# Optimization experiments

Measured on AMD Instinct MI355X. Metric: run time of the kernel, lower is better.

Reference implementation:

```python
import jax, jax.numpy as jnp
import numpy as np

EPS = 1e-5
BT_BATCH = 32       # BarlowTwinsLoss init batch_size (divides c)
BT_LAMBD = 0.005

def seg_sum(v, idx, n):
    return jax.ops.segment_sum(v, idx, num_segments=n)

def seg_mean(v, idx, n):
    s = seg_sum(v, idx, n)
    c = seg_sum(jnp.ones((v.shape[0],), v.dtype), idx, n)
    return s / jnp.maximum(c, 1.0)[:, None]

def gcn_conv(x, W, b, edge_index):
    n = x.shape[0]
    src, dst = edge_index[0], edge_index[1]
    xw = x @ W
    deg = 1.0 + seg_sum(jnp.ones(src.shape, x.dtype), dst, n)  # self-loop included
    norm = jax.lax.rsqrt(deg[src] * deg[dst])
    out = seg_sum(norm[:, None] * xw[src], dst, n) + xw / deg[:, None]
    return out + b

def barlow(z1, z2):
    # z-score with unbiased std (torch.std), then BatchNorm1d(affine=False) stats
    def std1(z):
        return (z - z.mean(0)) / jnp.std(z, axis=0, ddof=1)
    def bn(z):
        return (z - z.mean(0)) / jnp.sqrt(z.var(0) + EPS)
    a, b = bn(std1(z1)), bn(std1(z2))
    c = (a.T @ b) / BT_BATCH
    d = jnp.diagonal(c)
    on_diag = jnp.sum((d - 1.0) ** 2)
    off_diag = jnp.sum(c ** 2) - jnp.sum(d ** 2)
    return on_diag + BT_LAMBD * off_diag

def layernorm(t, g, b):
    m = t.mean(-1, keepdims=True)
    v = t.var(-1, keepdims=True)
    return g * (t - m) / jnp.sqrt(v + EPS) + b

def setup_inputs() -> dict:
    key = jax.random.key(0)
    ks = jax.random.split(key, 24)
    N, M, d, B = 50000, 10000, 128, 32
    NNZ, EG, EE = 200000, 600000, 160000
    s = 1.0 / np.sqrt(d)
    inp = {
        'x': jax.random.normal(ks[0], (N, d), jnp.float32),
        'hyperedge_feature': jax.random.normal(ks[1], (M, d), jnp.float32),
        'node_coord': jax.random.normal(ks[2], (N, 3), jnp.float32),
        'hyperedge_node_idx': jax.random.randint(ks[3], (NNZ,), 0, N),
        'hyperedge_edge_idx': jax.random.randint(ks[4], (NNZ,), 0, M),
        'node_batch_idx': jnp.sort(jax.random.randint(ks[5], (N,), 0, B)),
        'hyperedge_batch_idx': jnp.sort(jax.random.randint(ks[6], (M,), 0, B)),
        'X_X': jax.random.randint(ks[7], (2, EG), 0, N),
        'E_E': jax.random.randint(ks[8], (2, EE), 0, M),
        'num_graphs': B,
        'Wv': jax.random.normal(ks[9], (d, d), jnp.float32) * s,
        'bv': jnp.zeros((d,), jnp.float32),
        'We': jax.random.normal(ks[10], (d, d), jnp.float32) * s,
        'be': jnp.zeros((d,), jnp.float32),
        'Wx': jax.random.normal(ks[11], (d, d), jnp.float32) * s,
        'bx': jnp.zeros((d,), jnp.float32),
        'Weg': jax.random.normal(ks[12], (d, d), jnp.float32) * s,
        'beg': jnp.zeros((d,), jnp.float32),
        'ln_g': jnp.ones((d,), jnp.float32),
        'ln_b': jnp.zeros((d,), jnp.float32),
        'Wf': jax.random.normal(ks[13], (2 * d, d), jnp.float32) * (1.0 / np.sqrt(2 * d)),
        'bf': jnp.zeros((d,), jnp.float32),
    }
    return inp

def reference(x, hyperedge_feature, node_coord, hyperedge_node_idx, hyperedge_edge_idx,
              node_batch_idx, hyperedge_batch_idx, X_X, E_E, num_graphs,
              Wv, bv, We, be, Wx, bx, Weg, beg, ln_g, ln_b, Wf, bf):
    N, d = x.shape
    M = hyperedge_feature.shape[0]
    ni, ei = hyperedge_node_idx, hyperedge_edge_idx
    # E_HypergraphConv: node<->hyperedge bipartite message passing + EGNN-style coord update
    xw = x @ Wv + bv                     # [N, d]
    ew = hyperedge_feature @ We + be     # [M, d]
    e_conv = seg_mean(xw[ni], ei, M)     # hyperedge update from member nodes
    z_conv = seg_mean(ew[ei], ni, N)     # node update from incident hyperedges
    edge_coord = seg_mean(node_coord[ni], ei, M)          # [M, 3]
    rel = node_coord[ni] - edge_coord[ei]                 # [nnz, 3]
    phi = jnp.tanh(jnp.sum(xw[ni] * ew[ei], -1, keepdims=True)
                   * jax.lax.rsqrt(jnp.asarray(float(d), x.dtype)))
    update_coord = node_coord + seg_mean(rel * phi, ni, N)
    # implicit graph branches
    z_imp = gcn_conv(x, Wx, bx, X_X)
    e_imp = gcn_conv(hyperedge_feature, Weg, beg, E_E)
    bt_loss = barlow(z_imp, z_conv) + barlow(e_imp, e_conv)
    # norm -> GELU (erf, torch default) -> dropout(eval=identity) -> residual
    z = jax.nn.gelu(layernorm(z_conv, ln_g, ln_b), approximate=False) + x
    e = jax.nn.gelu(layernorm(e_conv, ln_g, ln_b), approximate=False) + hyperedge_feature
    z_graph = seg_mean(z, node_batch_idx, num_graphs)
    e_graph = seg_mean(e, hyperedge_batch_idx, num_graphs)
    graph = jnp.concatenate([z_graph, e_graph], axis=1) @ Wf + bf
    return z, e, update_coord, graph, bt_loss
```

## Files before the change

### kernel.cpp

```cpp
#include <hip/hip_runtime.h>
#include <hip/hip_bf16.h>

#define NB 32
#define GPN 448
#define GPM 80
#define RGRP 16

__device__ __forceinline__ float wave_sum(float v) {
#pragma unroll
  for (int off = 32; off; off >>= 1) v += __shfl_xor(v, off);
  return v;
}
__device__ __forceinline__ int wave_sum_i(int v) {
#pragma unroll
  for (int off = 32; off; off >>= 1) v += __shfl_xor(v, off);
  return v;
}

__device__ __forceinline__ float bf2f(unsigned short u) {
  return __uint_as_float(((unsigned int)u) << 16);
}
__device__ __forceinline__ unsigned short f2bf(float f) {
  unsigned int v = __float_as_uint(f);
  return (unsigned short)((v + 0x7FFFu + ((v >> 16) & 1u)) >> 16);
}

__global__ void count_kernel(const int* __restrict__ ni, const int* __restrict__ ei,
                             int nnz, const int* __restrict__ xx, int eg,
                             const int* __restrict__ ee, int eeN, int* cnt_n,
                             int* cnt_e, int* cnt_gx, int* cnt_ge, int* rank_pn,
                             int* rank_pe, int* rank_g, int* rank_h,
                             const float* __restrict__ coord, float* ec) {
  int i = blockIdx.x * 1024 + (int)threadIdx.x;
#pragma unroll
  for (int k = 0; k < 4; k++, i += 256) {
    if (i < nnz) {
      const int n = ni[i], e = ei[i];
      rank_pn[i] = atomicAdd(&cnt_n[n], 1);
      rank_pe[i] = atomicAdd(&cnt_e[e], 1);
      atomicAdd(&ec[e * 3 + 0], coord[n * 3 + 0]);
      atomicAdd(&ec[e * 3 + 1], coord[n * 3 + 1]);
      atomicAdd(&ec[e * 3 + 2], coord[n * 3 + 2]);
    } else if (i < nnz + eg) {
      const int j = i - nnz;
      rank_g[j] = atomicAdd(&cnt_gx[xx[eg + j]], 1);
    } else if (i < nnz + eg + eeN) {
      const int j = i - nnz - eg;
      rank_h[j] = atomicAdd(&cnt_ge[ee[eeN + j]], 1);
    }
  }
}

__device__ __forceinline__ void gemm_body(const float* __restrict__ X,
                                          const float* __restrict__ W1,
                                          const float* __restrict__ b1,
                                          unsigned short* __restrict__ out1,
                                          const float* __restrict__ W2,
                                          unsigned short* __restrict__ out2, int rows,
                                          int blk, unsigned short (*xs)[132]) {
  const int t = threadIdx.x;
  const int c4 = t & 31;
  const int rg = t >> 5;
  const int r0 = blk * 64;
#pragma unroll
  for (int i = 0; i < 8; i++) {
    const int idx = t + i * 256;
    const int row = idx >> 5, cc = idx & 31;
    const int gr = r0 + row;
    float4 v = make_float4(0.f, 0.f, 0.f, 0.f);
    if (gr < rows) v = ((const float4*)X)[(size_t)gr * 32 + cc];
    ushort4 u;
    u.x = f2bf(v.x); u.y = f2bf(v.y); u.z = f2bf(v.z); u.w = f2bf(v.w);
    *(ushort4*)&xs[row][cc * 4] = u;
  }
  __syncthreads();
  const float4* W1v = (const float4*)W1;
  const float4* W2v = (const float4*)W2;
  const float4 b4 = ((const float4*)b1)[c4];
  float4 acc1[8], acc2[8];
#pragma unroll
  for (int i = 0; i < 8; i++) {
    acc1[i] = b4;
    acc2[i] = make_float4(0.f, 0.f, 0.f, 0.f);
  }
  const int rbase = rg * 8;
#pragma unroll 2
  for (int k = 0; k < 128; k++) {
    const float4 w1 = W1v[k * 32 + c4];
    const float4 w2 = W2v[k * 32 + c4];
#pragma unroll
    for (int i = 0; i < 8; i++) {
      const float xv = bf2f(xs[rbase + i][k]);
      acc1[i].x = fmaf(xv, w1.x, acc1[i].x);
      acc1[i].y = fmaf(xv, w1.y, acc1[i].y);
      acc1[i].z = fmaf(xv, w1.z, acc1[i].z);
      acc1[i].w = fmaf(xv, w1.w, acc1[i].w);
      acc2[i].x = fmaf(xv, w2.x, acc2[i].x);
      acc2[i].y = fmaf(xv, w2.y, acc2[i].y);
      acc2[i].z = fmaf(xv, w2.z, acc2[i].z);
      acc2[i].w = fmaf(xv, w2.w, acc2[i].w);
    }
  }
#pragma unroll
  for (int i = 0; i < 8; i++) {
    const int gr = r0 + rbase + i;
    if (gr < rows) {
      ushort4 o1, o2;
      o1.x = f2bf(acc1[i].x); o1.y = f2bf(acc1[i].y);
      o1.z = f2bf(acc1[i].z); o1.w = f2bf(acc1[i].w);
      o2.x = f2bf(acc2[i].x); o2.y = f2bf(acc2[i].y);
      o2.z = f2bf(acc2[i].z); o2.w = f2bf(acc2[i].w);
      ((ushort4*)out1)[(size_t)gr * 32 + c4] = o1;
      ((ushort4*)out2)[(size_t)gr * 32 + c4] = o2;
    }
  }
}

__global__ __launch_bounds__(256) void scan_partial(
    const int* __restrict__ c0, int n0, const int* __restrict__ c1, int n1,
    const int* __restrict__ c2, int n2, const int* __restrict__ c3, int n3,
    int nb0, int nb1, int nb2, int nb3, int* __restrict__ bsums) {
  const int gb = blockIdx.x;
  const int* cnt;
  int lb, n;
  if (gb < nb0) { cnt = c0; lb = gb; n = n0; }
  else if (gb < nb0 + nb1) { cnt = c1; lb = gb - nb0; n = n1; }
  else if (gb < nb0 + nb1 + nb2) { cnt = c2; lb = gb - nb0 - nb1; n = n2; }
  else { cnt = c3; lb = gb - nb0 - nb1 - nb2; n = n3; }
  const int t = threadIdx.x;
  const int base = lb * 4096 + t * 16;
  int s = 0;
#pragma unroll
  for (int i = 0; i < 16; i++) {
    const int idx = base + i;
    if (idx < n) s += cnt[idx];
  }
  const int wsum = wave_sum_i(s);
  __shared__ int wsm[4];
  if ((t & 63) == 0) wsm[t >> 6] = wsum;
  __syncthreads();
  if (t == 0) bsums[gb] = wsm[0] + wsm[1] + wsm[2] + wsm[3];
}

__global__ void scan_bsums(const int* __restrict__ bsums, int nb0, int nb1, int nb2,
                           int nb3, int* __restrict__ bbase, int* __restrict__ totals) {
  if (threadIdx.x) return;
  int segs[4] = {nb0, nb1, nb2, nb3};
  int gb = 0;
  for (int a = 0; a < 4; a++) {
    int run = 0;
    for (int i = 0; i < segs[a]; i++) {
      bbase[gb] = run;
      run += bsums[gb];
      gb++;
    }
    totals[a] = run;
  }
}

__global__ __launch_bounds__(256) void scan_final(
    int* __restrict__ c0, int* rp0, float* rs0, float* ecd0, int n0,
    int* __restrict__ c1, int* rp1, float* rs1, float* ecd1, int n1,
    int* __restrict__ c2, int* rp2, float* rs2, float* ecd2, int n2,
    int* __restrict__ c3, int* rp3, float* rs3, float* ecd3, int n3,
    int nb0, int nb1, int nb2, int nb3, const int* __restrict__ bbase,
    const int* __restrict__ totals) {
  const int gb = blockIdx.x;
  int* cnt;
  int* rp;
  float* rs;
  float* ecd;
  int lb, n, a;
  if (gb < nb0) { cnt = c0; rp = rp0; rs = rs0; ecd = ecd0; lb = gb; n = n0; a = 0; }
  else if (gb < nb0 + nb1) { cnt = c1; rp = rp1; rs = rs1; ecd = ecd1; lb = gb - nb0; n = n1; a = 1; }
  else if (gb < nb0 + nb1 + nb2) { cnt = c2; rp = rp2; rs = rs2; ecd = ecd2; lb = gb - nb0 - nb1; n = n2; a = 2; }
  else { cnt = c3; rp = rp3; rs = rs3; ecd = ecd3; lb = gb - nb0 - nb1 - nb2; n = n3; a = 3; }
  const int t = threadIdx.x;
  const int base = lb * 4096 + t * 16;
  int vals[16];
  int s = 0;
#pragma unroll
  for (int i = 0; i < 16; i++) {
    const int idx = base + i;
    vals[i] = (idx < n) ? cnt[idx] : 0;
    s += vals[i];
  }
  __shared__ int tsum[256];
  tsum[t] = s;
  __syncthreads();
  for (int off = 1; off < 256; off <<= 1) {
    const int v = (t >= off) ? tsum[t - off] : 0;
    __syncthreads();
    tsum[t] += v;
    __syncthreads();
  }
  int run = bbase[gb] + (t ? tsum[t - 1] : 0);
#pragma unroll
  for (int i = 0; i < 16; i++) {
    const int idx = base + i;
    if (idx < n) {
      rp[idx] = run;
      if (rs) rs[idx] = rsqrtf(1.f + (float)vals[i]);
      if (ecd) {
        const float inv = 1.f / fmaxf((float)vals[i], 1.f);
        ecd[idx * 3 + 0] *= inv;
        ecd[idx * 3 + 1] *= inv;
        ecd[idx * 3 + 2] *= inv;
      }
      run += vals[i];
    }
  }
  if (t == 0 && lb == 0) rp[n] = totals[a];
}

__global__ __launch_bounds__(256) void fused_fill_gemm(
    const float* __restrict__ x, const float* __restrict__ Wv,
    const float* __restrict__ bv, unsigned short* __restrict__ xw,
    const float* __restrict__ Wx, unsigned short* __restrict__ xw2, int N, int nbGN,
    const float* __restrict__ hf, const float* __restrict__ We,
    const float* __restrict__ be, unsigned short* __restrict__ ew,
    const float* __restrict__ Weg, unsigned short* __restrict__ ew2, int M, int nbG,
    const int* __restrict__ ni, const int* __restrict__ ei, int nnz,
    const int* __restrict__ xx, int eg, const int* __restrict__ ee, int eeN,
    const int* __restrict__ rp_n, const int* __restrict__ rp_e,
    const int* __restrict__ rp_gx, const int* __restrict__ rp_ge,
    const int* __restrict__ rank_pn, const int* __restrict__ rank_pe,
    const int* __restrict__ rank_g, const int* __restrict__ rank_h, int* adj_n,
    int* adj_e, int* adj_gx, int* adj_ge, int nbFill, const int* __restrict__ nbi,
    int* cbn, const int* __restrict__ hbi, int* cbe) {
  __shared__ unsigned short xs[64][132];
  const int b = blockIdx.x;
  const int t = threadIdx.x;
  if (b < nbG) {
    if (b < nbGN)
      gemm_body(x, Wv, bv, xw, Wx, xw2, N, b, xs);
    else
      gemm_body(hf, We, be, ew, Weg, ew2, M, b - nbGN, xs);
    return;
  }
  const int fb = b - nbG;
  if (fb < nbFill) {
    int i = fb * 1024 + t;
#pragma unroll
    for (int k = 0; k < 4; k++, i += 256) {
      if (i < nnz) {
        const int n0 = ni[i], e0 = ei[i];
        adj_n[rp_n[n0] + rank_pn[i]] = e0;
        adj_e[rp_e[e0] + rank_pe[i]] = n0;
      } else if (i < nnz + eg) {
        const int j = i - nnz;
        adj_gx[rp_gx[xx[eg + j]] + rank_g[j]] = xx[j];
      } else if (i < nnz + eg + eeN) {
        const int j = i - nnz - eg;
        adj_ge[rp_ge[ee[eeN + j]] + rank_h[j]] = ee[j];
      }
    }
    return;
  }
  const bool B = (fb - nbFill) != 0;
  const int* idx = B ? hbi : nbi;
  const int nn = B ? M : N;
  int* out = B ? cbe : cbn;
  const int g = t;
  if (g >= NB) return;
  int lo = 0, hi = nn;
  while (lo < hi) { int mid = (lo + hi) >> 1; if (idx[mid] < g) lo = mid + 1; else hi = mid; }
  const int l = lo;
  lo = 0; hi = nn;
  while (lo < hi) { int mid = (lo + hi) >> 1; if (idx[mid] < g + 1) lo = mid + 1; else hi = mid; }
  out[g] = lo - l;
}

__device__ __forceinline__ void gcn_body(const unsigned short* __restrict__ xw,
                                         const int* __restrict__ rowptr,
                                         const int* __restrict__ adj,
                                         const float* __restrict__ rs,
                                         const float* __restrict__ bias,
                                         float* __restrict__ out, int n, int lb) {
  const int r = (lb * 256 + (int)threadIdx.x) >> 6;
  const int lane = threadIdx.x & 63;
  if (r >= n) return;
  const int lo = rowptr[r], hi = rowptr[r + 1];
  const float rd = rs[r];
  float2 acc = make_float2(0.f, 0.f);
  for (int base = lo; base < hi; base += 64) {
    const int mm = min(64, hi - base);
    int aj = 0;
    float rj = 0.f;
    if (base + lane < hi) {
      aj = adj[base + lane];
      rj = rs[aj];
    }
    for (int j = 0; j < mm; j++) {
      const int s = __shfl(aj, j);
      const float w = __shfl(rj, j);
      const ushort2 u = ((const ushort2*)xw)[(size_t)s * 64 + lane];
      acc.x = fmaf(w, bf2f(u.x), acc.x);
      acc.y = fmaf(w, bf2f(u.y), acc.y);
    }
  }
  const ushort2 su = ((const ushort2*)xw)[(size_t)r * 64 + lane];
  const float2 bb = ((const float2*)bias)[lane];
  float2 o;
  o.x = fmaf(rd, acc.x, fmaf(rd * rd, bf2f(su.x), bb.x));
  o.y = fmaf(rd, acc.y, fmaf(rd * rd, bf2f(su.y), bb.y));
  ((float2*)out)[(size_t)r * 64 + lane] = o;
}

__global__ __launch_bounds__(256) void fused_gathers(
    const unsigned short* __restrict__ ew, const unsigned short* __restrict__ xw,
    const float* __restrict__ coord, const float* __restrict__ ecoord,
    const int* __restrict__ rp_n, const int* __restrict__ adj_n,
    float* __restrict__ z_conv, float* __restrict__ outc, int N, int nbNode,
    const unsigned short* __restrict__ xw2, const int* __restrict__ rp_gx,
    const int* __restrict__ adj_gx, const float* __restrict__ rs_gx,
    const float* __restrict__ bx, float* __restrict__ outz, int nbGcnN,
    const unsigned short* __restrict__ ew2, const int* __restrict__ rp_ge,
    const int* __restrict__ adj_ge, const float* __restrict__ rs_ge,
    const float* __restrict__ beg, float* __restrict__ oute, int M, int nbGcnM,
    const int* __restrict__ rp_e, const int* __restrict__ adj_e,
    float* __restrict__ e_conv) {
  const int b = blockIdx.x;
  const int t = threadIdx.x;
  const int lane = t & 63;
  if (b < nbNode) {
    const int r = (b * 256 + t) >> 6;
    if (r >= N) return;
    const int lo = rp_n[r], hi = rp_n[r + 1];
    const ushort2 au = ((const ushort2*)xw)[(size_t)r * 64 + lane];
    const float2 a = make_float2(bf2f(au.x), bf2f(au.y));
    const float myc = (lane < 3) ? coord[r * 3 + lane] : 0.f;
    float2 acc = make_float2(0.f, 0.f);
    float cacc = 0.f;
    for (int base = lo; base < hi; base += 64) {
      const int mm = min(64, hi - base);
      int aj = (base + lane < hi) ? adj_n[base + lane] : 0;
      for (int j = 0; j < mm; j++) {
        const int e = __shfl(aj, j);
        const ushort2 bu = ((const ushort2*)ew)[(size_t)e * 64 + lane];
        const float2 bb = make_float2(bf2f(bu.x), bf2f(bu.y));
        acc.x += bb.x;
        acc.y += bb.y;
        const float dot = wave_sum(fmaf(a.x, bb.x, a.y * bb.y));
        const float ph = tanhf(dot * 0.08838834764831845f);
        if (lane < 3) cacc = fmaf(myc - ecoord[e * 3 + lane], ph, cacc);
      }
    }
    const float inv = 1.f / fmaxf((float)(hi - lo), 1.f);
    ((float2*)z_conv)[(size_t)r * 64 + lane] = make_float2(acc.x * inv, acc.y * inv);
    if (lane < 3) outc[r * 3 + lane] = myc + cacc * inv;
    return;
  }
  if (b < nbNode + nbGcnN) {
    gcn_body(xw2, rp_gx, adj_gx, rs_gx, bx, outz, N, b - nbNode);
    return;
  }
  if (b < nbNode + nbGcnN + nbGcnM) {
    gcn_body(ew2, rp_ge, adj_ge, rs_ge, beg, oute, M, b - nbNode - nbGcnN);
    return;
  }
  const int lb = b - nbNode - nbGcnN - nbGcnM;
  const int e = (lb * 256 + t) >> 6;
  if (e >= M) return;
  const int lo = rp_e[e], hi = rp_e[e + 1];
  float2 acc = make_float2(0.f, 0.f);
  for (int base = lo; base < hi; base += 64) {
    const int mm = min(64, hi - base);
    int aj = (base + lane < hi) ? adj_e[base + lane] : 0;
    for (int j = 0; j < mm; j++) {
      const int nidx = __shfl(aj, j);
      const ushort2 vu = ((const ushort2*)xw)[(size_t)nidx * 64 + lane];
      acc.x += bf2f(vu.x);
      acc.y += bf2f(vu.y);
    }
  }
  const float inv = 1.f / fmaxf((float)(hi - lo), 1.f);
  ((float2*)e_conv)[(size_t)e * 64 + lane] = make_float2(acc.x * inv, acc.y * inv);
}

__global__ __launch_bounds__(256) void gram_partial2(
    const float* __restrict__ Z1a, const float* __restrict__ Z2a, int na,
    float* __restrict__ parta, const float* __restrict__ Z1b,
    const float* __restrict__ Z2b, int nbm, float* __restrict__ partb,
    float* __restrict__ st, int nblkA) {
  const bool A = (int)blockIdx.x < nblkA;
  const int pid = A ? blockIdx.x : blockIdx.x - nblkA;
  const float* Z1 = A ? Z1a : Z1b;
  const float* Z2 = A ? Z2a : Z2b;
  const int n = A ? na : nbm;
  const int gparts = A ? GPN : GPM;
  float* part = (A ? parta : partb) + (size_t)pid * 16384;
  float* sum1 = st + (A ? 0 : 512);
  float* ssq1 = sum1 + 128;
  float* sum2 = sum1 + 256;
  float* ssq2 = sum1 + 384;
  __shared__ float4 s1[256], s2[256];
  const int t = threadIdx.x;
  const int ti = t >> 4, tj = t & 15;
  const int rpb = (n + gparts - 1) / gparts;
  const int lo = pid * rpb, hi = min(lo + rpb, n);
  float acc[8][8];
#pragma unroll
  for (int i = 0; i < 8; i++)
#pragma unroll
    for (int j = 0; j < 8; j++) acc[i][j] = 0.f;
  float cs = 0.f, cq = 0.f;
  const float* s1f = (const float*)s1;
  const float* s2f = (const float*)s2;
  const int c = t & 127;
  const bool low = t < 128;
  for (int rb = lo; rb < hi; rb += 8) {
    const int nr = min(8, hi - rb);
    __syncthreads();
    if (t < nr * 32) {
      const int rr = rb + (t >> 5);
      s1[t] = ((const float4*)Z1)[(size_t)rr * 32 + (t & 31)];
      s2[t] = ((const float4*)Z2)[(size_t)rr * 32 + (t & 31)];
    }
    __syncthreads();
    for (int r = 0; r < nr; r++) {
      const float4 a0 = s1[r * 32 + ti * 2], a1 = s1[r * 32 + ti * 2 + 1];
      const float4 b0 = s2[r * 32 + tj * 2], b1 = s2[r * 32 + tj * 2 + 1];
      const float av[8] = {a0.x, a0.y, a0.z, a0.w, a1.x, a1.y, a1.z, a1.w};
      const float bv[8] = {b0.x, b0.y, b0.z, b0.w, b1.x, b1.y, b1.z, b1.w};
#pragma unroll
      for (int i = 0; i < 8; i++)
#pragma unroll
        for (int j = 0; j < 8; j++) acc[i][j] = fmaf(av[i], bv[j], acc[i][j]);
      const float v = low ? s1f[r * 128 + c] : s2f[r * 128 + c];
      cs += v;
      cq = fmaf(v, v, cq);
    }
  }
  float4* P = (float4*)part;
#pragma unroll
  for (int i = 0; i < 8; i++) {
    P[(ti * 8 + i) * 32 + tj * 2] = make_float4(acc[i][0], acc[i][1], acc[i][2], acc[i][3]);
    P[(ti * 8 + i) * 32 + tj * 2 + 1] = make_float4(acc[i][4], acc[i][5], acc[i][6], acc[i][7]);
  }
  if (low) {
    atomicAdd(&sum1[c], cs);
    atomicAdd(&ssq1[c], cq);
  } else {
    atomicAdd(&sum2[c], cs);
    atomicAdd(&ssq2[c], cq);
  }
}

__global__ __launch_bounds__(256) void fused_reduce_ln(
    const float* __restrict__ parta, float* __restrict__ G1,
    const float* __restrict__ partb, float* __restrict__ G2,
    const float* __restrict__ convA, const float* __restrict__ residA,
    float* __restrict__ outA, int nA, int lnA, const float* __restrict__ convB,
    const float* __restrict__ residB, float* __restrict__ outB, int nBm,
    const float* __restrict__ g, const float* __restrict__ bvec) {
  const int b = blockIdx.x;
  const int t = threadIdx.x;
  const int NRED = (GPN / RGRP + GPM / RGRP) * 16;
  if (b < NRED) {
    const int nga = GPN / RGRP;
    const int slice = b & 15;
    const int grp = b >> 4;
    const bool A = grp < nga;
    const float* part = A ? parta : partb;
    float* G = A ? G1 : G2;
    const int g0 = (A ? grp : grp - nga) * RGRP;
    const int e = slice * 1024 + t * 4;
    float4 s = make_float4(0.f, 0.f, 0.f, 0.f);
#pragma unroll 4
    for (int p = 0; p < RGRP; p++) {
      const float4 v = *(const float4*)&part[(size_t)(g0 + p) * 16384 + e];
      s.x += v.x;
      s.y += v.y;
      s.z += v.z;
      s.w += v.w;
    }
    atomicAdd(&G[e], s.x);
    atomicAdd(&G[e + 1], s.y);
    atomicAdd(&G[e + 2], s.z);
    atomicAdd(&G[e + 3], s.w);
    return;
  }
  const int b2 = b - NRED;
  const bool A = b2 < lnA;
  const int lb = A ? b2 : b2 - lnA;
  const float* conv = A ? convA : convB;
  const float* resid = A ? residA : residB;
  float* out = A ? outA : outB;
  const int rows = A ? nA : nBm;
  const int w = (lb * 256 + t) >> 6;
  const int lane = t & 63;
  if (w >= rows) return;
  const float2 v = ((const float2*)conv)[(size_t)w * 64 + lane];
  const float m = wave_sum(v.x + v.y) * (1.f / 128.f);
  const float q = wave_sum(fmaf(v.x, v.x, v.y * v.y)) * (1.f / 128.f);
  const float rstd = rsqrtf(q - m * m + 1e-5f);
  const float2 gg = ((const float2*)g)[lane];
  const float2 bb = ((const float2*)bvec)[lane];
  const float2 rr = ((const float2*)resid)[(size_t)w * 64 + lane];
  float y0 = fmaf(gg.x, (v.x - m) * rstd, bb.x);
  float y1 = fmaf(gg.y, (v.y - m) * rstd, bb.y);
  y0 = 0.5f * y0 * (1.f + erff(y0 * 0.7071067811865476f));
  y1 = 0.5f * y1 * (1.f + erff(y1 * 0.7071067811865476f));
  float2 o;
  o.x = y0 + rr.x;
  o.y = y1 + rr.y;
  ((float2*)out)[(size_t)w * 64 + lane] = o;
}

__global__ __launch_bounds__(256) void fused_fin_pool(
    const float* __restrict__ G1, const float* __restrict__ G2,
    const float* __restrict__ st, float nA, float nB, float* outbt,
    const float* __restrict__ ZA, const int* __restrict__ bidxA, int n, int spA,
    float* poolA, const float* __restrict__ ZB, const int* __restrict__ bidxB, int m,
    float* poolB) {
  __shared__ float s1s[128], m1s[128], s2s[128], m2s[128];
  __shared__ float red[256];
  const int b = blockIdx.x;
  const int t = threadIdx.x;
  if (b < 2) {
    const bool A = b == 0;
    const float* G = A ? G1 : G2;
    const float* sum1 = st + (A ? 0 : 512);
    const float* ssq1 = sum1 + 128;
    const float* sum2 = sum1 + 256;
    const float* ssq2 = sum1 + 384;
    const float nn = A ? nA : nB;
    if (t < 128) {
      const float inv_n = 1.f / nn;
      const float bnf = (nn - 1.f) * inv_n + 1e-5f;
      float mu = sum1[t] * inv_n;
      float vu = (ssq1[t] * inv_n - mu * mu) * nn / (nn - 1.f);
      s1s[t] = rsqrtf(vu * bnf);
      m1s[t] = mu;
      mu = sum2[t] * inv_n;
      vu = (ssq2[t] * inv_n - mu * mu) * nn / (nn - 1.f);
      s2s[t] = rsqrtf(vu * bnf);
      m2s[t] = mu;
    }
    __syncthreads();
    float on = 0.f, off = 0.f;
    for (int idx = t; idx < 16384; idx += 256) {
      const int i = idx >> 7, j = idx & 127;
      const float c = s1s[i] * s2s[j] * (G[idx] - nn * m1s[i] * m2s[j]) * (1.f / 32.f);
      if (i == j) {
        const float dd = c - 1.f;
        on += dd * dd;
      } else {
        off += c * c;
      }
    }
    red[t] = on + 0.005f * off;
    __syncthreads();
    for (int s = 128; s; s >>= 1) {
      if (t < s) red[t] += red[t + s];
      __syncthreads();
    }
    if (t == 0) atomicAdd(outbt, red[0]);
    return;
  }
  const int pb = b - 2;
  const bool A = pb < spA;
  const int lb = A ? pb : pb - spA;
  const float* Z = A ? ZA : ZB;
  const int* bidx = A ? bidxA : bidxB;
  const int n2 = A ? n : m;
  float* pool = A ? poolA : poolB;
  const int c = t & 127;
  const int h = t >> 7;
  const int r0 = lb * 128 + h * 64;
  const int re = min(lb * 128 + (h + 1) * 64, n2);
  if (r0 >= n2) return;
  float acc = 0.f;
  int cur = bidx[r0];
  for (int r = r0; r < re; r++) {
    const int bb = bidx[r];
    if (bb != cur) {
      atomicAdd(&pool[cur * 128 + c], acc);
      acc = 0.f;
      cur = bb;
    }
    acc += Z[(size_t)r * 128 + c];
  }
  atomicAdd(&pool[cur * 128 + c], acc);
}

__global__ __launch_bounds__(128) void graph_gemm(
    const float* __restrict__ zg, const float* __restrict__ eg,
    const int* __restrict__ cnz, const int* __restrict__ cne,
    const float* __restrict__ Wf, const float* __restrict__ bf, float* out) {
  __shared__ float cat[256];
  const int g = blockIdx.x, t = threadIdx.x;
  cat[t] = zg[g * 128 + t] / fmaxf((float)cnz[g], 1.f);
  cat[128 + t] = eg[g * 128 + t] / fmaxf((float)cne[g], 1.f);
  __syncthreads();
  float acc = bf[t];
#pragma unroll 8
  for (int k = 0; k < 256; k++) acc = fmaf(cat[k], Wf[k * 128 + t], acc);
  out[g * 128 + t] = acc;
}

extern "C" void kernel_launch(void* const* d_in, const int* in_sizes, int n_in,
                              void* d_out, int out_size, void* d_ws, size_t ws_size,
                              hipStream_t stream) {
  const float* x = (const float*)d_in[0];
  const float* hf = (const float*)d_in[1];
  const float* coord = (const float*)d_in[2];
  const int* ni = (const int*)d_in[3];
  const int* ei = (const int*)d_in[4];
  const int* nb = (const int*)d_in[5];
  const int* hb = (const int*)d_in[6];
  const int* xx = (const int*)d_in[7];
  const int* ee = (const int*)d_in[8];
  const float* Wv = (const float*)d_in[10];
  const float* bv = (const float*)d_in[11];
  const float* We = (const float*)d_in[12];
  const float* be = (const float*)d_in[13];
  const float* Wx = (const float*)d_in[14];
  const float* bx = (const float*)d_in[15];
  const float* Weg = (const float*)d_in[16];
  const float* beg = (const float*)d_in[17];
  const float* lng = (const float*)d_in[18];
  const float* lnb = (const float*)d_in[19];
  const float* Wf = (const float*)d_in[20];
  const float* bf = (const float*)d_in[21];

  const int N = in_sizes[0] / 128;
  const int M = in_sizes[1] / 128;
  const int NNZ = in_sizes[3];
  const int EG = in_sizes[7] / 2;
  const int EE = in_sizes[8] / 2;

  float* ws = (float*)d_ws;
  size_t o = 0;
  unsigned short* xw = (unsigned short*)(ws + o);  o += (size_t)N * 64;
  unsigned short* ew = (unsigned short*)(ws + o);  o += (size_t)M * 64;
  unsigned short* xw2 = (unsigned short*)(ws + o); o += (size_t)N * 64;
  unsigned short* ew2 = (unsigned short*)(ws + o); o += (size_t)M * 64;
  int* rank_pn = (int*)(ws + o); o += NNZ;
  int* rank_pe = (int*)(ws + o); o += NNZ;
  int* rank_g = (int*)(ws + o);  o += EG;
  int* rank_h = (int*)(ws + o);  o += EE;
  float* z_conv = ws + o; o += (size_t)N * 128;
  float* e_conv = ws + o; o += (size_t)M * 128;
  float* rs_gx = ws + o;  o += N;
  float* rs_ge = ws + o;  o += M;
  const size_t fz0 = o;
  float* ecoord = ws + o; o += (size_t)M * 3;
  float* G1 = ws + o;     o += 16384;
  float* G2 = ws + o;     o += 16384;
  float* st = ws + o;     o += 1024;
  float* zg = ws + o;     o += NB * 128;
  float* eg_p = ws + o;   o += NB * 128;
  const size_t fz1 = o;
  int* wsi = (int*)(ws + o);
  size_t oi = 0;
  int* cnt_n = wsi + oi;  oi += N;
  int* cnt_e = wsi + oi;  oi += M;
  int* cnt_gx = wsi + oi; oi += N;
  int* cnt_ge = wsi + oi; oi += M;
  const size_t iz1 = oi;
  int* rp_n = wsi + oi;   oi += N + 1;
  int* rp_e = wsi + oi;   oi += M + 1;
  int* rp_gx = wsi + oi;  oi += N + 1;
  int* rp_ge = wsi + oi;  oi += M + 1;
  int* adj_n = wsi + oi;  oi += NNZ;
  int* adj_e = wsi + oi;  oi += NNZ;
  int* adj_gx = wsi + oi; oi += EG;
  int* adj_ge = wsi + oi; oi += EE;
  int* cbn = wsi + oi;    oi += NB;
  int* cbe = wsi + oi;    oi += NB;
  int* bsums = wsi + oi;  oi += 64;
  int* bbase = wsi + oi;  oi += 64;
  int* totals = wsi + oi; oi += 4;

  float* gpartA = ws;
  float* gpartB = ws + (size_t)GPN * 16384;

  float* outz = (float*)d_out;
  float* oute = outz + (size_t)N * 128;
  float* outc = oute + (size_t)M * 128;
  float* outg = outc + (size_t)N * 3;
  float* outbt = outg + NB * 128;

  hipMemsetAsync(ws + fz0, 0, (fz1 - fz0) * 4, stream);
  hipMemsetAsync(wsi, 0, iz1 * 4, stream);
  hipMemsetAsync(outbt, 0, 4, stream);

  const int tot = NNZ + EG + EE;
  const int nbCnt = (tot + 1023) >> 10;
  count_kernel<<<nbCnt, 256, 0, stream>>>(ni, ei, NNZ, xx, EG, ee, EE, cnt_n, cnt_e,
                                          cnt_gx, cnt_ge, rank_pn, rank_pe, rank_g,
                                          rank_h, coord, ecoord);

  const int nb0 = (N + 4095) >> 12, nb1 = (M + 4095) >> 12;
  const int sgrid = 2 * nb0 + 2 * nb1;
  scan_partial<<<sgrid, 256, 0, stream>>>(cnt_n, N, cnt_e, M, cnt_gx, N, cnt_ge, M,
                                          nb0, nb1, nb0, nb1, bsums);
  scan_bsums<<<1, 64, 0, stream>>>(bsums, nb0, nb1, nb0, nb1, bbase, totals);
  scan_final<<<sgrid, 256, 0, stream>>>(
      cnt_n, rp_n, nullptr, nullptr, N, cnt_e, rp_e, nullptr, ecoord, M, cnt_gx,
      rp_gx, rs_gx, nullptr, N, cnt_ge, rp_ge, rs_ge, nullptr, M, nb0, nb1, nb0, nb1,
      bbase, totals);

  const int nbGN = (N + 63) / 64, nbGM = (M + 63) / 64;
  const int nbG = nbGN + nbGM;
  const int nbFill = (tot + 1023) >> 10;
  fused_fill_gemm<<<nbG + nbFill + 2, 256, 0, stream>>>(
      x, Wv, bv, xw, Wx, xw2, N, nbGN, hf, We, be, ew, Weg, ew2, M, nbG, ni, ei, NNZ,
      xx, EG, ee, EE, rp_n, rp_e, rp_gx, rp_ge, rank_pn, rank_pe, rank_g, rank_h,
      adj_n, adj_e, adj_gx, adj_ge, nbFill, nb, cbn, hb, cbe);

  const int nbNode = (N + 3) / 4, nbGcnN = (N + 3) / 4, nbGcnM = (M + 3) / 4,
            nbHedge = (M + 3) / 4;
  fused_gathers<<<nbNode + nbGcnN + nbGcnM + nbHedge, 256, 0, stream>>>(
      ew, xw, coord, ecoord, rp_n, adj_n, z_conv, outc, N, nbNode, xw2, rp_gx, adj_gx,
      rs_gx, bx, outz, nbGcnN, ew2, rp_ge, adj_ge, rs_ge, beg, oute, M, nbGcnM, rp_e,
      adj_e, e_conv);

  gram_partial2<<<GPN + GPM, 256, 0, stream>>>(outz, z_conv, N, gpartA, oute, e_conv,
                                               M, gpartB, st, GPN);

  const int lnA = (N + 3) / 4;
  fused_reduce_ln<<<(GPN / RGRP + GPM / RGRP) * 16 + lnA + (M + 3) / 4, 256, 0,
                    stream>>>(gpartA, G1, gpartB, G2, z_conv, x, outz, N, lnA, e_conv,
                              hf, oute, M, lng, lnb);

  const int spA = (N + 127) / 128, spB = (M + 127) / 128;
  fused_fin_pool<<<2 + spA + spB, 256, 0, stream>>>(G1, G2, st, (float)N, (float)M,
                                                    outbt, outz, nb, N, spA, zg, oute,
                                                    hb, M, eg_p);

  graph_gemm<<<NB, 128, 0, stream>>>(zg, eg_p, cbn, cbe, Wf, bf, outg);
}
```

Baseline: 387.8 us.

## Use half-wave rows with 8-byte loads in gathers; compute edge coords by CSR gather

```diff
diff --git a/kernel.cpp b/kernel.cpp
--- a/kernel.cpp
+++ b/kernel.cpp
@@ -11,6 +11,11 @@
   for (int off = 32; off; off >>= 1) v += __shfl_xor(v, off);
   return v;
 }
+__device__ __forceinline__ float half_sum(float v) {
+#pragma unroll
+  for (int off = 16; off; off >>= 1) v += __shfl_xor(v, off);
+  return v;
+}
 __device__ __forceinline__ int wave_sum_i(int v) {
 #pragma unroll
   for (int off = 32; off; off >>= 1) v += __shfl_xor(v, off);
@@ -29,8 +34,7 @@
                              int nnz, const int* __restrict__ xx, int eg,
                              const int* __restrict__ ee, int eeN, int* cnt_n,
                              int* cnt_e, int* cnt_gx, int* cnt_ge, int* rank_pn,
-                             int* rank_pe, int* rank_g, int* rank_h,
-                             const float* __restrict__ coord, float* ec) {
+                             int* rank_pe, int* rank_g, int* rank_h) {
   int i = blockIdx.x * 1024 + (int)threadIdx.x;
 #pragma unroll
   for (int k = 0; k < 4; k++, i += 256) {
@@ -38,9 +42,6 @@
       const int n = ni[i], e = ei[i];
       rank_pn[i] = atomicAdd(&cnt_n[n], 1);
       rank_pe[i] = atomicAdd(&cnt_e[e], 1);
-      atomicAdd(&ec[e * 3 + 0], coord[n * 3 + 0]);
-      atomicAdd(&ec[e * 3 + 1], coord[n * 3 + 1]);
-      atomicAdd(&ec[e * 3 + 2], coord[n * 3 + 2]);
     } else if (i < nnz + eg) {
       const int j = i - nnz;
       rank_g[j] = atomicAdd(&cnt_gx[xx[eg + j]], 1);
@@ -159,22 +160,21 @@
 }
 
 __global__ __launch_bounds__(256) void scan_final(
-    int* __restrict__ c0, int* rp0, float* rs0, float* ecd0, int n0,
-    int* __restrict__ c1, int* rp1, float* rs1, float* ecd1, int n1,
-    int* __restrict__ c2, int* rp2, float* rs2, float* ecd2, int n2,
-    int* __restrict__ c3, int* rp3, float* rs3, float* ecd3, int n3,
+    int* __restrict__ c0, int* rp0, float* rs0, int n0,
+    int* __restrict__ c1, int* rp1, float* rs1, int n1,
+    int* __restrict__ c2, int* rp2, float* rs2, int n2,
+    int* __restrict__ c3, int* rp3, float* rs3, int n3,
     int nb0, int nb1, int nb2, int nb3, const int* __restrict__ bbase,
     const int* __restrict__ totals) {
   const int gb = blockIdx.x;
   int* cnt;
   int* rp;
   float* rs;
-  float* ecd;
   int lb, n, a;
-  if (gb < nb0) { cnt = c0; rp = rp0; rs = rs0; ecd = ecd0; lb = gb; n = n0; a = 0; }
-  else if (gb < nb0 + nb1) { cnt = c1; rp = rp1; rs = rs1; ecd = ecd1; lb = gb - nb0; n = n1; a = 1; }
-  else if (gb < nb0 + nb1 + nb2) { cnt = c2; rp = rp2; rs = rs2; ecd = ecd2; lb = gb - nb0 - nb1; n = n2; a = 2; }
-  else { cnt = c3; rp = rp3; rs = rs3; ecd = ecd3; lb = gb - nb0 - nb1 - nb2; n = n3; a = 3; }
+  if (gb < nb0) { cnt = c0; rp = rp0; rs = rs0; lb = gb; n = n0; a = 0; }
+  else if (gb < nb0 + nb1) { cnt = c1; rp = rp1; rs = rs1; lb = gb - nb0; n = n1; a = 1; }
+  else if (gb < nb0 + nb1 + nb2) { cnt = c2; rp = rp2; rs = rs2; lb = gb - nb0 - nb1; n = n2; a = 2; }
+  else { cnt = c3; rp = rp3; rs = rs3; lb = gb - nb0 - nb1 - nb2; n = n3; a = 3; }
   const int t = threadIdx.x;
   const int base = lb * 4096 + t * 16;
   int vals[16];
@@ -201,12 +201,6 @@
     if (idx < n) {
       rp[idx] = run;
       if (rs) rs[idx] = rsqrtf(1.f + (float)vals[i]);
-      if (ecd) {
-        const float inv = 1.f / fmaxf((float)vals[i], 1.f);
-        ecd[idx * 3 + 0] *= inv;
-        ecd[idx * 3 + 1] *= inv;
-        ecd[idx * 3 + 2] *= inv;
-      }
       run += vals[i];
     }
   }
@@ -271,20 +265,39 @@
   out[g] = lo - l;
 }
 
+__global__ __launch_bounds__(256) void ecoord_gather(
+    const float* __restrict__ coord, const int* __restrict__ rp_e,
+    const int* __restrict__ adj_e, float* __restrict__ ecoord, int m) {
+  const int e = (blockIdx.x * 256 + (int)threadIdx.x) >> 6;
+  const int lane = threadIdx.x & 63;
+  if (e >= m) return;
+  const int lo = rp_e[e], hi = rp_e[e + 1];
+  float cacc = 0.f;
+  for (int base = lo; base < hi; base += 64) {
+    const int mm = min(64, hi - base);
+    int aj = (base + lane < hi) ? adj_e[base + lane] : 0;
+    for (int j = 0; j < mm; j++) {
+      const int nidx = __shfl(aj, j);
+      if (lane < 3) cacc += coord[nidx * 3 + lane];
+    }
+  }
+  if (lane < 3) ecoord[e * 3 + lane] = cacc / fmaxf((float)(hi - lo), 1.f);
+}
+
 __device__ __forceinline__ void gcn_body(const unsigned short* __restrict__ xw,
                                          const int* __restrict__ rowptr,
                                          const int* __restrict__ adj,
                                          const float* __restrict__ rs,
                                          const float* __restrict__ bias,
                                          float* __restrict__ out, int n, int lb) {
-  const int r = (lb * 256 + (int)threadIdx.x) >> 6;
-  const int lane = threadIdx.x & 63;
+  const int r = (lb * 256 + (int)threadIdx.x) >> 5;
+  const int lane = threadIdx.x & 31;
   if (r >= n) return;
   const int lo = rowptr[r], hi = rowptr[r + 1];
   const float rd = rs[r];
-  float2 acc = make_float2(0.f, 0.f);
-  for (int base = lo; base < hi; base += 64) {
-    const int mm = min(64, hi - base);
+  float4 acc = make_float4(0.f, 0.f, 0.f, 0.f);
+  for (int base = lo; base < hi; base += 32) {
+    const int mm = min(32, hi - base);
     int aj = 0;
     float rj = 0.f;
     if (base + lane < hi) {
@@ -292,19 +305,23 @@
       rj = rs[aj];
     }
     for (int j = 0; j < mm; j++) {
-      const int s = __shfl(aj, j);
-      const float w = __shfl(rj, j);
-      const ushort2 u = ((const ushort2*)xw)[(size_t)s * 64 + lane];
+      const int s = __shfl(aj, j, 32);
+      const float w = __shfl(rj, j, 32);
+      const ushort4 u = ((const ushort4*)xw)[(size_t)s * 32 + lane];
       acc.x = fmaf(w, bf2f(u.x), acc.x);
       acc.y = fmaf(w, bf2f(u.y), acc.y);
-    }
-  }
-  const ushort2 su = ((const ushort2*)xw)[(size_t)r * 64 + lane];
-  const float2 bb = ((const float2*)bias)[lane];
-  float2 o;
+      acc.z = fmaf(w, bf2f(u.z), acc.z);
+      acc.w = fmaf(w, bf2f(u.w), acc.w);
+    }
+  }
+  const ushort4 su = ((const ushort4*)xw)[(size_t)r * 32 + lane];
+  const float4 bb = ((const float4*)bias)[lane];
+  float4 o;
   o.x = fmaf(rd, acc.x, fmaf(rd * rd, bf2f(su.x), bb.x));
   o.y = fmaf(rd, acc.y, fmaf(rd * rd, bf2f(su.y), bb.y));
-  ((float2*)out)[(size_t)r * 64 + lane] = o;
+  o.z = fmaf(rd, acc.z, fmaf(rd * rd, bf2f(su.z), bb.z));
+  o.w = fmaf(rd, acc.w, fmaf(rd * rd, bf2f(su.w), bb.w));
+  ((float4*)out)[(size_t)r * 32 + lane] = o;
 }
 
 __global__ __launch_bounds__(256) void fused_gathers(
@@ -322,32 +339,40 @@
     float* __restrict__ e_conv) {
   const int b = blockIdx.x;
   const int t = threadIdx.x;
-  const int lane = t & 63;
+  const int lane = t & 31;
   if (b < nbNode) {
-    const int r = (b * 256 + t) >> 6;
+    const int r = (b * 256 + t) >> 5;
     if (r >= N) return;
     const int lo = rp_n[r], hi = rp_n[r + 1];
-    const ushort2 au = ((const ushort2*)xw)[(size_t)r * 64 + lane];
-    const float2 a = make_float2(bf2f(au.x), bf2f(au.y));
+    const ushort4 au = ((const ushort4*)xw)[(size_t)r * 32 + lane];
+    const float a0 = bf2f(au.x), a1 = bf2f(au.y), a2 = bf2f(au.z), a3 = bf2f(au.w);
     const float myc = (lane < 3) ? coord[r * 3 + lane] : 0.f;
-    float2 acc = make_float2(0.f, 0.f);
+    float4 acc = make_float4(0.f, 0.f, 0.f, 0.f);
     float cacc = 0.f;
-    for (int base = lo; base < hi; base += 64) {
-      const int mm = min(64, hi - base);
+    for (int base = lo; base < hi; base += 32) {
+      const int mm = min(32, hi - base);
       int aj = (base + lane < hi) ? adj_n[base + lane] : 0;
       for (int j = 0; j < mm; j++) {
-        const int e = __shfl(aj, j);
-        const ushort2 bu = ((const ushort2*)ew)[(size_t)e * 64 + lane];
-        const float2 bb = make_float2(bf2f(bu.x), bf2f(bu.y));
-        acc.x += bb.x;
-        acc.y += bb.y;
-        const float dot = wave_sum(fmaf(a.x, bb.x, a.y * bb.y));
+        const int e = __shfl(aj, j, 32);
+        const ushort4 bu = ((const ushort4*)ew)[(size_t)e * 32 + lane];
+        const float b0 = bf2f(bu.x), b1 = bf2f(bu.y), b2 = bf2f(bu.z), b3 = bf2f(bu.w);
+        acc.x += b0;
+        acc.y += b1;
+        acc.z += b2;
+        acc.w += b3;
+        float dot = fmaf(a0, b0, fmaf(a1, b1, fmaf(a2, b2, a3 * b3)));
+        dot = half_sum(dot);
         const float ph = tanhf(dot * 0.08838834764831845f);
         if (lane < 3) cacc = fmaf(myc - ecoord[e * 3 + lane], ph, cacc);
       }
     }
     const float inv = 1.f / fmaxf((float)(hi - lo), 1.f);
-    ((float2*)z_conv)[(size_t)r * 64 + lane] = make_float2(acc.x * inv, acc.y * inv);
+    float4 o;
+    o.x = acc.x * inv;
+    o.y = acc.y * inv;
+    o.z = acc.z * inv;
+    o.w = acc.w * inv;
+    ((float4*)z_conv)[(size_t)r * 32 + lane] = o;
     if (lane < 3) outc[r * 3 + lane] = myc + cacc * inv;
     return;
   }
@@ -360,22 +385,29 @@
     return;
   }
   const int lb = b - nbNode - nbGcnN - nbGcnM;
-  const int e = (lb * 256 + t) >> 6;
+  const int e = (lb * 256 + t) >> 5;
   if (e >= M) return;
   const int lo = rp_e[e], hi = rp_e[e + 1];
-  float2 acc = make_float2(0.f, 0.f);
-  for (int base = lo; base < hi; base += 64) {
-    const int mm = min(64, hi - base);
+  float4 acc = make_float4(0.f, 0.f, 0.f, 0.f);
+  for (int base = lo; base < hi; base += 32) {
+    const int mm = min(32, hi - base);
     int aj = (base + lane < hi) ? adj_e[base + lane] : 0;
     for (int j = 0; j < mm; j++) {
-      const int nidx = __shfl(aj, j);
-      const ushort2 vu = ((const ushort2*)xw)[(size_t)nidx * 64 + lane];
+      const int nidx = __shfl(aj, j, 32);
+      const ushort4 vu = ((const ushort4*)xw)[(size_t)nidx * 32 + lane];
       acc.x += bf2f(vu.x);
       acc.y += bf2f(vu.y);
+      acc.z += bf2f(vu.z);
+      acc.w += bf2f(vu.w);
     }
   }
   const float inv = 1.f / fmaxf((float)(hi - lo), 1.f);
-  ((float2*)e_conv)[(size_t)e * 64 + lane] = make_float2(acc.x * inv, acc.y * inv);
+  float4 o;
+  o.x = acc.x * inv;
+  o.y = acc.y * inv;
+  o.z = acc.z * inv;
+  o.w = acc.w * inv;
+  ((float4*)e_conv)[(size_t)e * 32 + lane] = o;
 }
 
 __global__ __launch_bounds__(256) void gram_partial2(
@@ -645,8 +677,8 @@
   float* e_conv = ws + o; o += (size_t)M * 128;
   float* rs_gx = ws + o;  o += N;
   float* rs_ge = ws + o;  o += M;
+  float* ecoord = ws + o; o += (size_t)M * 3;
   const size_t fz0 = o;
-  float* ecoord = ws + o; o += (size_t)M * 3;
   float* G1 = ws + o;     o += 16384;
   float* G2 = ws + o;     o += 16384;
   float* st = ws + o;     o += 1024;
@@ -691,17 +723,16 @@
   const int nbCnt = (tot + 1023) >> 10;
   count_kernel<<<nbCnt, 256, 0, stream>>>(ni, ei, NNZ, xx, EG, ee, EE, cnt_n, cnt_e,
                                           cnt_gx, cnt_ge, rank_pn, rank_pe, rank_g,
-                                          rank_h, coord, ecoord);
+                                          rank_h);
 
   const int nb0 = (N + 4095) >> 12, nb1 = (M + 4095) >> 12;
   const int sgrid = 2 * nb0 + 2 * nb1;
   scan_partial<<<sgrid, 256, 0, stream>>>(cnt_n, N, cnt_e, M, cnt_gx, N, cnt_ge, M,
                                           nb0, nb1, nb0, nb1, bsums);
   scan_bsums<<<1, 64, 0, stream>>>(bsums, nb0, nb1, nb0, nb1, bbase, totals);
-  scan_final<<<sgrid, 256, 0, stream>>>(
-      cnt_n, rp_n, nullptr, nullptr, N, cnt_e, rp_e, nullptr, ecoord, M, cnt_gx,
-      rp_gx, rs_gx, nullptr, N, cnt_ge, rp_ge, rs_ge, nullptr, M, nb0, nb1, nb0, nb1,
-      bbase, totals);
+  scan_final<<<sgrid, 256, 0, stream>>>(cnt_n, rp_n, nullptr, N, cnt_e, rp_e, nullptr,
+                                        M, cnt_gx, rp_gx, rs_gx, N, cnt_ge, rp_ge,
+                                        rs_ge, M, nb0, nb1, nb0, nb1, bbase, totals);
 
   const int nbGN = (N + 63) / 64, nbGM = (M + 63) / 64;
   const int nbG = nbGN + nbGM;
@@ -711,8 +742,10 @@
       xx, EG, ee, EE, rp_n, rp_e, rp_gx, rp_ge, rank_pn, rank_pe, rank_g, rank_h,
       adj_n, adj_e, adj_gx, adj_ge, nbFill, nb, cbn, hb, cbe);
 
-  const int nbNode = (N + 3) / 4, nbGcnN = (N + 3) / 4, nbGcnM = (M + 3) / 4,
-            nbHedge = (M + 3) / 4;
+  ecoord_gather<<<(M + 3) / 4, 256, 0, stream>>>(coord, rp_e, adj_e, ecoord, M);
+
+  const int nbNode = (N + 7) / 8, nbGcnN = (N + 7) / 8, nbGcnM = (M + 7) / 8,
+            nbHedge = (M + 7) / 8;
   fused_gathers<<<nbNode + nbGcnN + nbGcnM + nbHedge, 256, 0, stream>>>(
       ew, xw, coord, ecoord, rp_n, adj_n, z_conv, outc, N, nbNode, xw2, rp_gx, adj_gx,
       rs_gx, bx, outz, nbGcnN, ew2, rp_ge, adj_ge, rs_ge, beg, oute, M, nbGcnM, rp_e,
```

Measured after the change: 332.4 us. 14.3% less time.
